# Optimization experiments

Measured on AMD Instinct MI355X. Metric: run time of the kernel, lower is better.

The kernel has to match this reference:

```python
import jax, jax.numpy as jnp
import numpy as np

N = 8192
IN_F = 512
OUT_F = 64
NEG_SLOPE = 0.01  # nn.LeakyReLU default
MASK_VAL = -1e9


def setup_inputs() -> dict:
    key = jax.random.key(0)
    k_h, k_adj, k_W, k_a = jax.random.split(key, 4)
    h = jax.random.normal(k_h, (N, IN_F), dtype=jnp.float32)
    adjacency = jax.random.randint(k_adj, (N, N), 0, 2, dtype=jnp.int32)
    # xavier_uniform bounds
    bW = float(np.sqrt(6.0 / (IN_F + OUT_F)))
    ba = float(np.sqrt(6.0 / (2 * OUT_F + 1)))
    W = jax.random.uniform(k_W, (IN_F, OUT_F), minval=-bW, maxval=bW, dtype=jnp.float32)
    a = jax.random.uniform(k_a, (2 * OUT_F, 1), minval=-ba, maxval=ba, dtype=jnp.float32)
    return {"h": h, "adjacency": adjacency, "W": W, "a": a}


def reference(h, adjacency, W, a):
    WH = h @ W                                  # [N, out_f]
    wh1 = WH @ a[:OUT_F, :]                     # [N, 1]
    wh2 = WH @ a[OUT_F:, :]                     # [N, 1]
    e = jax.nn.leaky_relu(wh1 + wh2.T, negative_slope=NEG_SLOPE)  # [N, N]
    attnt = jnp.where(adjacency > 0, e, jnp.float32(MASK_VAL))
    attnt = jax.nn.softmax(attnt, axis=1)       # row-wise softmax
    hfirst = attnt @ WH                         # [N, out_f]
    return jax.nn.elu(hfirst)
```

## Files before the change

kernel.cpp:

```cpp
#include <hip/hip_runtime.h>
#include <hip/hip_bf16.h>

#define N 8192
#define IN_F 512
#define OUT_F 64
#define S_SPLIT 16
#define JT (N / S_SPLIT)
#define NB (N / 8)
#define LDP 520

typedef __attribute__((ext_vector_type(8))) short short8;
typedef __attribute__((ext_vector_type(4))) float floatx4;
typedef __attribute__((ext_vector_type(4))) int intx4;

__device__ inline short f2bf(float x) {
    __hip_bfloat16 b = __float2bfloat16(x);
    return __builtin_bit_cast(short, b);
}

__global__ __launch_bounds__(256) void k_pack(const int* __restrict__ adj,
                                              unsigned* __restrict__ mask) {
    int wv = (blockIdx.x * 256 + threadIdx.x) >> 6;
    int lane = threadIdx.x & 63;
    const int* p = adj + (size_t)wv * 512 + lane;
    unsigned long long m0 = __ballot(p[0]   > 0);
    unsigned long long m1 = __ballot(p[64]  > 0);
    unsigned long long m2 = __ballot(p[128] > 0);
    unsigned long long m3 = __ballot(p[192] > 0);
    unsigned long long m4 = __ballot(p[256] > 0);
    unsigned long long m5 = __ballot(p[320] > 0);
    unsigned long long m6 = __ballot(p[384] > 0);
    unsigned long long m7 = __ballot(p[448] > 0);
    if (lane < 16) {
        unsigned long long s0 = (lane & 2) ? m1 : m0;
        unsigned long long s1 = (lane & 2) ? m3 : m2;
        unsigned long long s2 = (lane & 2) ? m5 : m4;
        unsigned long long s3 = (lane & 2) ? m7 : m6;
        unsigned long long t0 = (lane & 4) ? s1 : s0;
        unsigned long long t1 = (lane & 4) ? s3 : s2;
        unsigned long long u  = (lane & 8) ? t1 : t0;
        unsigned dw = (lane & 1) ? (unsigned)(u >> 32) : (unsigned)u;
        mask[wv * 16 + lane] = dw;
    }
}

__global__ void k_wt(const float* __restrict__ W, short* __restrict__ WT) {
    int idx = blockIdx.x * 256 + threadIdx.x;
    int k = idx >> 6, f = idx & 63;
    WT[f * IN_F + k] = f2bf(W[k * OUT_F + f]);
}

__global__ __launch_bounds__(64) void k_wh(const float* __restrict__ h,
                                           const short* __restrict__ WT,
                                           const float* __restrict__ a,
                                           short* __restrict__ WHbT,
                                           float* __restrict__ wh1,
                                           float* __restrict__ wh2) {
    __shared__ float tile[OUT_F][17];
    int lane = threadIdx.x;
    int n = lane & 15, q = lane >> 4;
    int i0 = blockIdx.x * 16;
    int rowA = i0 + n;
    const float* hp = h + (size_t)rowA * IN_F + q * 8;
    floatx4 acc[4] = {};
    for (int k0 = 0; k0 < IN_F; k0 += 32) {
        floatx4 h0 = *(const floatx4*)(hp + k0);
        floatx4 h1 = *(const floatx4*)(hp + k0 + 4);
        short8 af;
#pragma unroll
        for (int j = 0; j < 4; j++) { af[j] = f2bf(h0[j]); af[j + 4] = f2bf(h1[j]); }
#pragma unroll
        for (int b = 0; b < 4; b++) {
            short8 bf_ = *(const short8*)(WT + (b * 16 + n) * IN_F + k0 + q * 8);
            acc[b] = __builtin_amdgcn_mfma_f32_16x16x32_bf16(af, bf_, acc[b], 0, 0, 0);
        }
    }
#pragma unroll
    for (int b = 0; b < 4; b++)
#pragma unroll
        for (int r = 0; r < 4; r++)
            tile[b * 16 + n][q * 4 + r] = acc[b][r];
    float a1v[4], a2v[4];
#pragma unroll
    for (int b = 0; b < 4; b++) { a1v[b] = a[b * 16 + n]; a2v[b] = a[OUT_F + b * 16 + n]; }
#pragma unroll
    for (int r = 0; r < 4; r++) {
        float s1 = 0.f, s2 = 0.f;
#pragma unroll
        for (int b = 0; b < 4; b++) { s1 += acc[b][r] * a1v[b]; s2 += acc[b][r] * a2v[b]; }
#pragma unroll
        for (int m = 1; m <= 8; m <<= 1) {
            s1 += __shfl_xor(s1, m, 64);
            s2 += __shfl_xor(s2, m, 64);
        }
        if (n == 0) {
            wh1[i0 + q * 4 + r] = s1;
            wh2[i0 + q * 4 + r] = s2;
        }
    }
    __syncthreads();
    const float* tc = tile[lane];
    short8 s0, s1v;
#pragma unroll
    for (int k = 0; k < 8; k++) { s0[k] = f2bf(tc[k]); s1v[k] = f2bf(tc[k + 8]); }
    *(short8*)(WHbT + (size_t)lane * N + i0) = s0;
    *(short8*)(WHbT + (size_t)lane * N + i0 + 8) = s1v;
}

__global__ __launch_bounds__(256, 2) void k_attn(const unsigned char* __restrict__ mask,
                                                 const short* __restrict__ WHbT,
                                                 const float* __restrict__ wh1,
                                                 const float* __restrict__ wh2,
                                                 float* __restrict__ num_part,
                                                 float* __restrict__ den_part) {
    __shared__ short ldsb[OUT_F * LDP];
    int tid = threadIdx.x;
    int w = tid >> 6;
    int lane = tid & 63;
    int n = lane & 15, q = lane >> 4;
    int split = blockIdx.y;
    int j0 = split * JT;
    int i0 = blockIdx.x * 256 + w * 64;

#pragma unroll
    for (int l = 0; l < 16; l++) {
        int idx = l * 256 + tid;
        int f = idx >> 6, c16 = idx & 63;
        short8 v = *(const short8*)(WHbT + (size_t)f * N + j0 + c16 * 8);
        *(short8*)(ldsb + f * LDP + c16 * 8) = v;
    }
    __syncthreads();

    float wh1f[4];
#pragma unroll
    for (int rf = 0; rf < 4; rf++) wh1f[rf] = wh1[i0 + rf * 16 + n];

    floatx4 acc[4][4] = {};
    float dsum[4] = {0.f, 0.f, 0.f, 0.f};
    const float* w2p = wh2 + j0 + q * 8;
    const short* lp = ldsb + q * 8;
    int qs = q * 8;

    intx4 mcur[4], mnxt[4];
#pragma unroll
    for (int rf = 0; rf < 4; rf++)
        mcur[rf] = *(const intx4*)(mask + (size_t)(i0 + rf * 16 + n) * NB + split * 64);

    for (int g = 0; g < 4; g++) {
        if (g < 3) {
#pragma unroll
            for (int rf = 0; rf < 4; rf++)
                mnxt[rf] = *(const intx4*)(mask + (size_t)(i0 + rf * 16 + n) * NB
                                           + split * 64 + (g + 1) * 16);
        }
#pragma unroll
        for (int d = 0; d < 4; d++) {
            int s = g * 4 + d;
            floatx4 w20 = *(const floatx4*)(w2p + s * 32);
            floatx4 w21 = *(const floatx4*)(w2p + s * 32 + 4);
            short8 bfr[4];
#pragma unroll
            for (int b = 0; b < 4; b++)
                bfr[b] = *(const short8*)(lp + (b * 16 + n) * LDP + s * 32);
#pragma unroll
            for (int rf = 0; rf < 4; rf++) {
                unsigned md = (unsigned)mcur[rf][d];
                float p[8];
#pragma unroll
                for (int jj = 0; jj < 8; jj++) {
                    float e = wh1f[rf] + ((jj < 4) ? w20[jj] : w21[jj - 4]);
                    float el = fmaxf(e, 0.01f * e);
                    float pv = __expf(el);
                    pv = ((md >> (qs + jj)) & 1u) ? pv : 0.f;
                    p[jj] = pv;
                    dsum[rf] += pv;
                }
                short8 af;
#pragma unroll
                for (int jj = 0; jj < 8; jj++) af[jj] = f2bf(p[jj]);
#pragma unroll
                for (int b = 0; b < 4; b++)
                    acc[rf][b] = __builtin_amdgcn_mfma_f32_16x16x32_bf16(af, bfr[b], acc[rf][b], 0, 0, 0);
            }
        }
#pragma unroll
        for (int rf = 0; rf < 4; rf++) mcur[rf] = mnxt[rf];
    }

#pragma unroll
    for (int rf = 0; rf < 4; rf++) {
        float d = dsum[rf];
        d += __shfl_xor(d, 16, 64);
        d += __shfl_xor(d, 32, 64);
        if (q == 0) den_part[(size_t)split * N + i0 + rf * 16 + n] = d;
    }

    float* np_ = num_part + (size_t)split * N * OUT_F;
#pragma unroll
    for (int rf = 0; rf < 4; rf++)
#pragma unroll
        for (int b = 0; b < 4; b++)
#pragma unroll
            for (int r = 0; r < 4; r++)
                np_[(size_t)(i0 + rf * 16 + q * 4 + r) * OUT_F + b * 16 + n] = acc[rf][b][r];
}

__global__ void k_final(const float* __restrict__ num_part,
                        const float* __restrict__ den_part,
                        float* __restrict__ out) {
    int idx = blockIdx.x * 256 + threadIdx.x;
    int row = idx >> 6;
    float s = 0.f, d = 0.f;
#pragma unroll
    for (int sp = 0; sp < S_SPLIT; sp++) {
        s += num_part[(size_t)sp * N * OUT_F + idx];
        d += den_part[sp * N + row];
    }
    float x = s / d;
    out[idx] = (x > 0.f) ? x : (__expf(x) - 1.f);
}

extern "C" void kernel_launch(void* const* d_in, const int* in_sizes, int n_in,
                              void* d_out, int out_size, void* d_ws, size_t ws_size,
                              hipStream_t stream) {
    const float* h = (const float*)d_in[0];
    const int* adj = (const int*)d_in[1];
    const float* W = (const float*)d_in[2];
    const float* a = (const float*)d_in[3];
    float* out = (float*)d_out;

    char* ws = (char*)d_ws;
    short* WHbT     = (short*)(ws);
    short* WT       = (short*)(ws + (size_t)(1 << 20));
    float* wh1      = (float*)(ws + (size_t)(1 << 20) + (64 << 10));
    float* wh2      = wh1 + N;
    unsigned* maskb = (unsigned*)(ws + (size_t)(2 << 20));
    float* num_p    = (float*)(ws + (size_t)(16 << 20));
    float* den_p    = (float*)(ws + (size_t)(48 << 20));

    k_pack<<<dim3((N / 32) * (N / 256) * 4), dim3(256), 0, stream>>>(adj, maskb);
    k_wt<<<dim3(128), dim3(256), 0, stream>>>(W, WT);
    k_wh<<<dim3(N / 16), dim3(64), 0, stream>>>(h, WT, a, WHbT, wh1, wh2);
    k_attn<<<dim3(N / 256, S_SPLIT), dim3(256), 0, stream>>>((const unsigned char*)maskb,
                                                             WHbT, wh1, wh2, num_p, den_p);
    k_final<<<dim3((N * OUT_F) / 256), dim3(256), 0, stream>>>(num_p, den_p, out);
}
```

Before: 411.8 us.

## Fuse adjacency mask reading into attention kernel and compute denominators via MFMA

Removes the separate bit-packing kernel and has the attention kernel read the int32 adjacency matrix directly, using software-pipelined double-buffered loads. The row-sum denominator now comes from an extra MFMA against a ones vector instead of scalar adds and shuffles. Exp is switched to exp2 with log2e folded into wh1/wh2, and the LDS pitch and k_wh loop unrolling are adjusted. Each attention block now reads 32-bit adjacency values instead of packed bits. Because of the 16-way split, adjacency traffic now lands on the attention kernel's critical path rather than a single streaming pass.

```diff
diff --git a/kernel.cpp b/kernel.cpp
--- a/kernel.cpp
+++ b/kernel.cpp
@@ -6,8 +6,8 @@
 #define OUT_F 64
 #define S_SPLIT 16
 #define JT (N / S_SPLIT)
-#define NB (N / 8)
-#define LDP 520
+#define LDP 536
+#define LOG2E 1.44269504088896340736f
 
 typedef __attribute__((ext_vector_type(8))) short short8;
 typedef __attribute__((ext_vector_type(4))) float floatx4;
@@ -18,30 +18,12 @@
     return __builtin_bit_cast(short, b);
 }
 
-__global__ __launch_bounds__(256) void k_pack(const int* __restrict__ adj,
-                                              unsigned* __restrict__ mask) {
-    int wv = (blockIdx.x * 256 + threadIdx.x) >> 6;
-    int lane = threadIdx.x & 63;
-    const int* p = adj + (size_t)wv * 512 + lane;
-    unsigned long long m0 = __ballot(p[0]   > 0);
-    unsigned long long m1 = __ballot(p[64]  > 0);
-    unsigned long long m2 = __ballot(p[128] > 0);
-    unsigned long long m3 = __ballot(p[192] > 0);
-    unsigned long long m4 = __ballot(p[256] > 0);
-    unsigned long long m5 = __ballot(p[320] > 0);
-    unsigned long long m6 = __ballot(p[384] > 0);
-    unsigned long long m7 = __ballot(p[448] > 0);
-    if (lane < 16) {
-        unsigned long long s0 = (lane & 2) ? m1 : m0;
-        unsigned long long s1 = (lane & 2) ? m3 : m2;
-        unsigned long long s2 = (lane & 2) ? m5 : m4;
-        unsigned long long s3 = (lane & 2) ? m7 : m6;
-        unsigned long long t0 = (lane & 4) ? s1 : s0;
-        unsigned long long t1 = (lane & 4) ? s3 : s2;
-        unsigned long long u  = (lane & 8) ? t1 : t0;
-        unsigned dw = (lane & 1) ? (unsigned)(u >> 32) : (unsigned)u;
-        mask[wv * 16 + lane] = dw;
-    }
+__device__ inline float fexp2(float x) {
+#if __has_builtin(__builtin_amdgcn_exp2f)
+    return __builtin_amdgcn_exp2f(x);
+#else
+    return exp2f(x);
+#endif
 }
 
 __global__ void k_wt(const float* __restrict__ W, short* __restrict__ WT) {
@@ -63,6 +45,7 @@
     int rowA = i0 + n;
     const float* hp = h + (size_t)rowA * IN_F + q * 8;
     floatx4 acc[4] = {};
+#pragma unroll
     for (int k0 = 0; k0 < IN_F; k0 += 32) {
         floatx4 h0 = *(const floatx4*)(hp + k0);
         floatx4 h1 = *(const floatx4*)(hp + k0 + 4);
@@ -94,8 +77,8 @@
             s2 += __shfl_xor(s2, m, 64);
         }
         if (n == 0) {
-            wh1[i0 + q * 4 + r] = s1;
-            wh2[i0 + q * 4 + r] = s2;
+            wh1[i0 + q * 4 + r] = s1 * LOG2E;
+            wh2[i0 + q * 4 + r] = s2 * LOG2E;
         }
     }
     __syncthreads();
@@ -107,7 +90,7 @@
     *(short8*)(WHbT + (size_t)lane * N + i0 + 8) = s1v;
 }
 
-__global__ __launch_bounds__(256, 2) void k_attn(const unsigned char* __restrict__ mask,
+__global__ __launch_bounds__(256, 2) void k_attn(const int* __restrict__ adj,
                                                  const short* __restrict__ WHbT,
                                                  const float* __restrict__ wh1,
                                                  const float* __restrict__ wh2,
@@ -136,64 +119,74 @@
     for (int rf = 0; rf < 4; rf++) wh1f[rf] = wh1[i0 + rf * 16 + n];
 
     floatx4 acc[4][4] = {};
-    float dsum[4] = {0.f, 0.f, 0.f, 0.f};
+    floatx4 accd[4] = {};
     const float* w2p = wh2 + j0 + q * 8;
     const short* lp = ldsb + q * 8;
-    int qs = q * 8;
-
-    intx4 mcur[4], mnxt[4];
+
+    short8 onesf = {};
+    if (n == 0) {
+        short o = f2bf(1.0f);
+#pragma unroll
+        for (int jj = 0; jj < 8; jj++) onesf[jj] = o;
+    }
+
+    const int* ap = adj + j0 + q * 8;
+    size_t roff[4];
+#pragma unroll
+    for (int rf = 0; rf < 4; rf++) roff[rf] = (size_t)(i0 + rf * 16 + n) * N;
+
+    intx4 A0[4], A1[4], B0[4], B1[4];
+
+    auto loads = [&](intx4* D0, intx4* D1, int s) {
+#pragma unroll
+        for (int rf = 0; rf < 4; rf++) {
+            const int* pp = ap + roff[rf] + s * 32;
+            D0[rf] = *(const intx4*)pp;
+            D1[rf] = *(const intx4*)(pp + 4);
+        }
+    };
+
+    auto step = [&](const intx4* D0, const intx4* D1, int s) {
+        floatx4 w20 = *(const floatx4*)(w2p + s * 32);
+        floatx4 w21 = *(const floatx4*)(w2p + s * 32 + 4);
+        short8 bfr[4];
+#pragma unroll
+        for (int b = 0; b < 4; b++)
+            bfr[b] = *(const short8*)(lp + (b * 16 + n) * LDP + s * 32);
+#pragma unroll
+        for (int rf = 0; rf < 4; rf++) {
+            float p[8];
+#pragma unroll
+            for (int jj = 0; jj < 8; jj++) {
+                float e = wh1f[rf] + ((jj < 4) ? w20[jj] : w21[jj - 4]);
+                float el = fmaxf(e, 0.01f * e);
+                int av = (jj < 4) ? D0[rf][jj] : D1[rf][jj - 4];
+                el = (av > 0) ? el : -1024.0f;
+                p[jj] = fexp2(el);
+            }
+            short8 af;
+#pragma unroll
+            for (int jj = 0; jj < 8; jj++) af[jj] = f2bf(p[jj]);
+#pragma unroll
+            for (int b = 0; b < 4; b++)
+                acc[rf][b] = __builtin_amdgcn_mfma_f32_16x16x32_bf16(af, bfr[b], acc[rf][b], 0, 0, 0);
+            accd[rf] = __builtin_amdgcn_mfma_f32_16x16x32_bf16(af, onesf, accd[rf], 0, 0, 0);
+        }
+    };
+
+    loads(A0, A1, 0);
+    for (int sp = 0; sp < 8; sp++) {
+        int s0 = sp * 2;
+        loads(B0, B1, s0 + 1);
+        step(A0, A1, s0);
+        loads(A0, A1, (s0 + 2) & 15);
+        step(B0, B1, s0 + 1);
+    }
+
 #pragma unroll
     for (int rf = 0; rf < 4; rf++)
-        mcur[rf] = *(const intx4*)(mask + (size_t)(i0 + rf * 16 + n) * NB + split * 64);
-
-    for (int g = 0; g < 4; g++) {
-        if (g < 3) {
-#pragma unroll
-            for (int rf = 0; rf < 4; rf++)
-                mnxt[rf] = *(const intx4*)(mask + (size_t)(i0 + rf * 16 + n) * NB
-                                           + split * 64 + (g + 1) * 16);
-        }
-#pragma unroll
-        for (int d = 0; d < 4; d++) {
-            int s = g * 4 + d;
-            floatx4 w20 = *(const floatx4*)(w2p + s * 32);
-            floatx4 w21 = *(const floatx4*)(w2p + s * 32 + 4);
-            short8 bfr[4];
-#pragma unroll
-            for (int b = 0; b < 4; b++)
-                bfr[b] = *(const short8*)(lp + (b * 16 + n) * LDP + s * 32);
-#pragma unroll
-            for (int rf = 0; rf < 4; rf++) {
-                unsigned md = (unsigned)mcur[rf][d];
-                float p[8];
-#pragma unroll
-                for (int jj = 0; jj < 8; jj++) {
-                    float e = wh1f[rf] + ((jj < 4) ? w20[jj] : w21[jj - 4]);
-                    float el = fmaxf(e, 0.01f * e);
-                    float pv = __expf(el);
-                    pv = ((md >> (qs + jj)) & 1u) ? pv : 0.f;
-                    p[jj] = pv;
-                    dsum[rf] += pv;
-                }
-                short8 af;
-#pragma unroll
-                for (int jj = 0; jj < 8; jj++) af[jj] = f2bf(p[jj]);
-#pragma unroll
-                for (int b = 0; b < 4; b++)
-                    acc[rf][b] = __builtin_amdgcn_mfma_f32_16x16x32_bf16(af, bfr[b], acc[rf][b], 0, 0, 0);
-            }
-        }
-#pragma unroll
-        for (int rf = 0; rf < 4; rf++) mcur[rf] = mnxt[rf];
-    }
-
-#pragma unroll
-    for (int rf = 0; rf < 4; rf++) {
-        float d = dsum[rf];
-        d += __shfl_xor(d, 16, 64);
-        d += __shfl_xor(d, 32, 64);
-        if (q == 0) den_part[(size_t)split * N + i0 + rf * 16 + n] = d;
-    }
+        if (n == 0)
+            *(floatx4*)(den_part + (size_t)split * N + i0 + rf * 16 + q * 4) = accd[rf];
 
     float* np_ = num_part + (size_t)split * N * OUT_F;
 #pragma unroll
@@ -234,14 +227,12 @@
     short* WT       = (short*)(ws + (size_t)(1 << 20));
     float* wh1      = (float*)(ws + (size_t)(1 << 20) + (64 << 10));
     float* wh2      = wh1 + N;
-    unsigned* maskb = (unsigned*)(ws + (size_t)(2 << 20));
     float* num_p    = (float*)(ws + (size_t)(16 << 20));
     float* den_p    = (float*)(ws + (size_t)(48 << 20));
 
-    k_pack<<<dim3((N / 32) * (N / 256) * 4), dim3(256), 0, stream>>>(adj, maskb);
     k_wt<<<dim3(128), dim3(256), 0, stream>>>(W, WT);
     k_wh<<<dim3(N / 16), dim3(64), 0, stream>>>(h, WT, a, WHbT, wh1, wh2);
-    k_attn<<<dim3(N / 256, S_SPLIT), dim3(256), 0, stream>>>((const unsigned char*)maskb,
-                                                             WHbT, wh1, wh2, num_p, den_p);
+    k_attn<<<dim3(N / 256, S_SPLIT), dim3(256), 0, stream>>>(adj, WHbT, wh1, wh2,
+                                                             num_p, den_p);
     k_final<<<dim3((N * OUT_F) / 256), dim3(256), 0, stream>>>(num_p, den_p, out);
 }
```

Result: no change. 406.2 us (-1.3%).
